# Optimization experiments

Hardware: AMD Instinct MI355X
Metric: run time of the kernel (lower is better)

The kernel has to match this reference:

```python
import jax, jax.numpy as jnp
import numpy as np

N_NODES = 50000
N_FEAT = 63          # nodeChannels C = N_FEAT + 1 = 64
N_EDGES = 800000
N_LABELS = 10000
BATCH = 4
N_LAYERS = 5
C = N_FEAT + 1


def setup_inputs() -> dict:
    key = jax.random.key(0)
    ks = jax.random.split(key, 16)
    s = 0.05  # small init scale for numerical sanity
    return {
        "cov": jax.random.normal(ks[0], (BATCH, N_LABELS), jnp.float32),
        "nodes": jax.random.normal(ks[1], (N_NODES, N_FEAT), jnp.float32),
        "edges": jax.random.randint(ks[2], (2, N_EDGES), 0, N_NODES, jnp.int64 if jax.config.jax_enable_x64 else jnp.int32),
        "count2label": jnp.arange(N_LABELS, dtype=jnp.int32),
        "ggc_weight": jax.random.normal(ks[3], (N_LAYERS, C, C), jnp.float32) * s,
        "gru_w_ih": jax.random.normal(ks[4], (3 * C, C), jnp.float32) * s,
        "gru_w_hh": jax.random.normal(ks[5], (3 * C, C), jnp.float32) * s,
        "gru_b_ih": jax.random.normal(ks[6], (3 * C,), jnp.float32) * s,
        "gru_b_hh": jax.random.normal(ks[7], (3 * C,), jnp.float32) * s,
        "ai_w": jax.random.normal(ks[8], (2 * C, 2 * C), jnp.float32) * s,
        "ai_b": jax.random.normal(ks[9], (2 * C,), jnp.float32) * s,
        "aj_w": jax.random.normal(ks[10], (2 * C, 2 * C), jnp.float32) * s,
        "aj_b": jax.random.normal(ks[11], (2 * C,), jnp.float32) * s,
        "mlp_w": jax.random.normal(ks[12], (256, 2 * C), jnp.float32) * s,
        "mlp_b": jax.random.normal(ks[13], (256,), jnp.float32) * s,
        "critic_w": jax.random.normal(ks[14], (1, 256), jnp.float32) * s,
        "critic_b": jax.random.normal(ks[15], (1,), jnp.float32) * s,
    }


def _gru_cell(m, h, w_ih, w_hh, b_ih, b_hh):
    # torch GRUCell, gate order r, z, n
    gx = m @ w_ih.T + b_ih   # [..., 3C]
    gh = h @ w_hh.T + b_hh
    c = h.shape[-1]
    xr, xz, xn = gx[..., :c], gx[..., c:2 * c], gx[..., 2 * c:]
    hr, hz, hn = gh[..., :c], gh[..., c:2 * c], gh[..., 2 * c:]
    r = jax.nn.sigmoid(xr + hr)
    z = jax.nn.sigmoid(xz + hz)
    n = jnp.tanh(xn + r * hn)
    return (1.0 - z) * n + z * h


def reference(cov, nodes, edges, count2label, ggc_weight,
              gru_w_ih, gru_w_hh, gru_b_ih, gru_b_hh,
              ai_w, ai_b, aj_w, aj_b, mlp_w, mlp_b, critic_w, critic_b):
    n, f = nodes.shape
    b = cov.shape[0]
    # scatter coverage into per-graph node channel: covInGraph[count2label] = cov
    cov_in_graph = jnp.zeros((b, n), cov.dtype).at[:, count2label].set(cov)
    # batched node input [B, N, C]; batched graph = B identical copies w/ offset edges
    x0 = jnp.concatenate(
        [jnp.broadcast_to(nodes, (b, n, f)), cov_in_graph[..., None]], axis=-1)
    src, dst = edges[0], edges[1]

    def scatter_add(mb):  # [N, C] -> [N, C]: sum messages from source at target
        return jax.ops.segment_sum(mb[src], dst, num_segments=n)

    x = x0
    for i in range(ggc_weight.shape[0]):
        m = x @ ggc_weight[i]                     # dense per-layer matmul [B,N,C]
        agg = jax.vmap(scatter_add)(m)            # edge scatter-add propagate
        x = _gru_cell(agg, x, gru_w_ih, gru_w_hh, gru_b_ih, gru_b_hh)

    # attention gate: sigmoid(Wi cat) * relu(Wj cat), cat = [x, x0]
    cat = jnp.concatenate([x, x0], axis=-1)       # [B, N, 2C]
    att = jax.nn.sigmoid(cat @ ai_w.T + ai_b) * jax.nn.relu(cat @ aj_w.T + aj_b)
    pooled = jax.nn.relu(att.sum(axis=1))         # global_add_pool -> [B, 2C]
    state = jax.nn.relu(pooled @ mlp_w.T + mlp_b) # graphmlp
    return state @ critic_w.T + critic_b          # critic value [B, 1]
```

## Files before the change

kernel.cpp:

```cpp
#include <hip/hip_runtime.h>
#include <math.h>

#define NN 50000
#define NF 63
#define NE 800000
#define NL 10000
#define NB 4
#define NLAY 5
#define BN (NB*NN)
#define NTILES (BN/64)
#define SCAN_NBLK ((NN+255)/256)
#define HIST_NBLK ((NE+255)/256)
#define X0_NBLK ((BN*16)/256)
#define COV_NBLK ((NB*NL+255)/256)

using f32x4  = __attribute__((ext_vector_type(4))) float;
using f32x2  = __attribute__((ext_vector_type(2))) float;
using bf16x8 = __attribute__((ext_vector_type(8))) __bf16;

__device__ __forceinline__ float frcp(float x){ return __builtin_amdgcn_rcpf(x); }
__device__ __forceinline__ float sigm(float v){ return frcp(1.f + __expf(-v)); }
__device__ __forceinline__ float tanh_f(float v){ return fmaf(-2.f, frcp(__expf(2.f*v) + 1.f), 1.f); }

__device__ __forceinline__ ushort f2bf(float f){
    uint u = __builtin_bit_cast(uint, f);
    u += 0x7fffu + ((u >> 16) & 1u);
    return (ushort)(u >> 16);
}
__device__ __forceinline__ float bf_lo(uint v){ return __builtin_bit_cast(float, v << 16); }
__device__ __forceinline__ float bf_hi(uint v){ return __builtin_bit_cast(float, v & 0xffff0000u); }
__device__ __forceinline__ float bfu(ushort v){ return __builtin_bit_cast(float, ((uint)v) << 16); }

__device__ __forceinline__ bf16x8 ldfrag(const ushort* p){
    uint4 v = *(const uint4*)p;
    return __builtin_bit_cast(bf16x8, v);
}
__device__ __forceinline__ f32x4 MFMA(bf16x8 a, bf16x8 b, f32x4 c){
    return __builtin_amdgcn_mfma_f32_16x16x32_bf16(a, b, c, 0, 0, 0);
}

__global__ void k_setup(const int* __restrict__ edges, int* __restrict__ cnt,
                        const float* __restrict__ wih, const float* __restrict__ whh,
                        const float* __restrict__ aiw, const float* __restrict__ ajw,
                        const float* __restrict__ ggc,
                        ushort* __restrict__ whhb, ushort* __restrict__ aiwb,
                        ushort* __restrict__ ajwb, ushort* __restrict__ wfb,
                        const float* __restrict__ nodes, ushort* __restrict__ x0I,
                        uchar* __restrict__ x0F){
    int bid = blockIdx.x;
    if (bid < HIST_NBLK){
        int e = bid*256 + threadIdx.x;
        if (e < NE) atomicAdd(&cnt[edges[NE + e]], 1);
        return;
    }
    if (bid < HIST_NBLK + 416){
        int i = (bid - HIST_NBLK)*256 + threadIdx.x;
        if (i < 12288)        whhb[i]        = f2bf(whh[i]);
        else if (i < 28672)   aiwb[i-12288]  = f2bf(aiw[i-12288]);
        else if (i < 45056)   ajwb[i-28672]  = f2bf(ajw[i-28672]);
        else if (i < 106496){
            int t = i - 45056;
            int lay = t / 12288;
            int rem = t % 12288;
            int n = rem >> 6, k = rem & 63;
            const float* W  = ggc + lay*4096 + k*64;
            const float* wr = wih + n*64;
            float s = 0.f;
            #pragma unroll 8
            for (int c = 0; c < 64; ++c) s = fmaf(W[c], wr[c], s);
            wfb[t] = f2bf(s);
        }
        return;
    }
    int f = (bid - HIST_NBLK - 416)*256 + threadIdx.x;
    int row = f >> 4, c4 = f & 15;
    int n = row % NN, b = row / NN;
    float v[4];
    #pragma unroll
    for (int i = 0; i < 4; ++i){
        int c = c4*4 + i;
        v[i] = (c < NF) ? nodes[(size_t)n*NF + c] : 0.f;
    }
    uint2 pk;
    pk.x = (uint)f2bf(v[0]) | ((uint)f2bf(v[1]) << 16);
    pk.y = (uint)f2bf(v[2]) | ((uint)f2bf(v[3]) << 16);
    *(uint2*)(x0I + ((size_t)n*4 + b)*64 + c4*4) = pk;
    if (b == 0){
        uint q = 0;
        q = (uint)__builtin_amdgcn_cvt_pk_fp8_f32(v[0], v[1], (int)q, false);
        q = (uint)__builtin_amdgcn_cvt_pk_fp8_f32(v[2], v[3], (int)q, true);
        *(uint*)(x0F + (size_t)n*64 + c4*4) = q;
    }
}

__global__ void k_scan1(const int* __restrict__ cnt, int* __restrict__ tmp, int* __restrict__ bsum,
                        const float* __restrict__ cov, const int* __restrict__ c2l,
                        ushort* __restrict__ x0I, ushort* __restrict__ covB){
    if (blockIdx.x >= SCAN_NBLK){
        int i = (blockIdx.x - SCAN_NBLK)*256 + threadIdx.x;
        if (i < NB*NL){
            int b = i / NL, j = i % NL;
            int nd = c2l[j];
            ushort vb = f2bf(cov[i]);
            x0I[((size_t)nd*4 + b)*64 + 63] = vb;
            covB[(size_t)nd*4 + b] = vb;
        }
        return;
    }
    __shared__ int sh[256];
    int tx = threadIdx.x, i = blockIdx.x*256 + tx;
    int v = (i < NN) ? cnt[i] : 0;
    sh[tx] = v; __syncthreads();
    for (int off = 1; off < 256; off <<= 1){
        int u = (tx >= off) ? sh[tx-off] : 0;
        __syncthreads();
        sh[tx] += u;
        __syncthreads();
    }
    int incl = sh[tx];
    if (i < NN) tmp[i] = incl - v;
    if (tx == 255) bsum[blockIdx.x] = incl;
}

__global__ void k_scan2(const int* __restrict__ bsum, int* __restrict__ boff){
    __shared__ int sh[256];
    int tx = threadIdx.x;
    int v = (tx < SCAN_NBLK) ? bsum[tx] : 0;
    sh[tx] = v; __syncthreads();
    for (int off = 1; off < 256; off <<= 1){
        int u = (tx >= off) ? sh[tx-off] : 0;
        __syncthreads();
        sh[tx] += u;
        __syncthreads();
    }
    boff[tx] = sh[tx] - v;
}

__global__ void k_scan3(const int* __restrict__ tmp, const int* __restrict__ boff,
                        int* __restrict__ row_start, int* __restrict__ cursor){
    int i = blockIdx.x*256 + threadIdx.x;
    if (i < NN){
        int rs = tmp[i] + boff[blockIdx.x];
        row_start[i] = rs;
        cursor[i] = rs;
    }
    if (i == 0) row_start[NN] = NE;
}

__global__ void k_fillcsr(const int* __restrict__ edges, int* __restrict__ cursor, int* __restrict__ csr_src){
    int e = blockIdx.x*256 + threadIdx.x;
    if (e < NE){
        int d = edges[NE + e];
        int pos = atomicAdd(&cursor[d], 1);
        csr_src[pos] = edges[e];
    }
}

__device__ __forceinline__ void gather0q(const uchar* __restrict__ x0F,
                                         const ushort* __restrict__ covB,
                                         const int* __restrict__ row_start,
                                         const int* __restrict__ csr_src,
                                         int d0, int l, ushort* __restrict__ sAgg,
                                         int rbase){
    const int qn = l >> 4, t = l & 15;
    const uint off = (uint)(t*4);
    const int d = d0 + qn;
    const int e0 = row_start[d], e1 = row_start[d+1];
    f32x2 a01 = (f32x2){0.f,0.f}, a23 = (f32x2){0.f,0.f};
    float c = 0.f;
    int e = e0;
    for (; e + 16 <= e1; e += 16){
        int s[16];
        #pragma unroll
        for (int j = 0; j < 16; ++j) s[j] = csr_src[e + j];
        uint v[16];
        #pragma unroll
        for (int j = 0; j < 16; ++j) v[j] = *(const uint*)(x0F + (size_t)s[j]*64 + off);
        #pragma unroll
        for (int j = 0; j < 16; ++j){
            a01 += __builtin_amdgcn_cvt_pk_f32_fp8(v[j], false);
            a23 += __builtin_amdgcn_cvt_pk_f32_fp8(v[j], true);
        }
        if (t < 4){
            #pragma unroll
            for (int j = 0; j < 16; ++j) c += bf_lo((uint)covB[(size_t)s[j]*4 + t]);
        }
    }
    if (e < e1){
        int s[16];
        #pragma unroll
        for (int j = 0; j < 16; ++j){ int ee = e + j; if (ee >= e1) ee = e1 - 1; s[j] = csr_src[ee]; }
        uint v[16];
        #pragma unroll
        for (int j = 0; j < 16; ++j){
            v[j] = *(const uint*)(x0F + (size_t)s[j]*64 + off);
            if (e + j >= e1) v[j] = 0u;
        }
        #pragma unroll
        for (int j = 0; j < 16; ++j){
            a01 += __builtin_amdgcn_cvt_pk_f32_fp8(v[j], false);
            a23 += __builtin_amdgcn_cvt_pk_f32_fp8(v[j], true);
        }
        if (t < 4){
            #pragma unroll
            for (int j = 0; j < 16; ++j){
                float cv = bf_lo((uint)covB[(size_t)s[j]*4 + t]);
                c += (e + j < e1) ? cv : 0.f;
            }
        }
    }
    uint2 pk;
    pk.x = (uint)f2bf(a01.x) | ((uint)f2bf(a01.y) << 16);
    pk.y = (uint)f2bf(a23.x) | ((uint)f2bf(a23.y) << 16);
    #pragma unroll
    for (int b = 0; b < 4; ++b){
        float cb = __shfl(c, (l & 48) | b);
        uint2 o = pk;
        if (t == 15) o.y = (o.y & 0xffffu) | ((uint)f2bf(cb) << 16);
        *(uint2*)(&sAgg[(size_t)(rbase + qn*4 + b)*72 + t*4]) = o;
    }
}

__device__ __forceinline__ void gather4q(const uchar* __restrict__ xF,
                                         const int* __restrict__ row_start,
                                         const int* __restrict__ csr_src,
                                         int d0, int l, ushort* __restrict__ sAgg,
                                         int rbase){
    const int qn = l >> 4;
    const int t  = l & 15;
    const uint off = (uint)(t*16);
    const int d = d0 + qn;
    const int e0 = row_start[d], e1 = row_start[d+1];
    f32x2 ac[8];
    #pragma unroll
    for (int k = 0; k < 8; ++k) ac[k] = (f32x2){0.f,0.f};

    int e = e0;
    for (; e + 16 <= e1; e += 16){
        int s[16];
        #pragma unroll
        for (int j = 0; j < 16; ++j) s[j] = csr_src[e + j];
        uint4 v[16];
        #pragma unroll
        for (int j = 0; j < 16; ++j) v[j] = *(const uint4*)(xF + (size_t)s[j]*256 + off);
        #pragma unroll
        for (int j = 0; j < 16; ++j){
            ac[0] += __builtin_amdgcn_cvt_pk_f32_fp8(v[j].x, false);
            ac[1] += __builtin_amdgcn_cvt_pk_f32_fp8(v[j].x, true);
            ac[2] += __builtin_amdgcn_cvt_pk_f32_fp8(v[j].y, false);
            ac[3] += __builtin_amdgcn_cvt_pk_f32_fp8(v[j].y, true);
            ac[4] += __builtin_amdgcn_cvt_pk_f32_fp8(v[j].z, false);
            ac[5] += __builtin_amdgcn_cvt_pk_f32_fp8(v[j].z, true);
            ac[6] += __builtin_amdgcn_cvt_pk_f32_fp8(v[j].w, false);
            ac[7] += __builtin_amdgcn_cvt_pk_f32_fp8(v[j].w, true);
        }
    }
    if (e < e1){
        int s[16];
        #pragma unroll
        for (int j = 0; j < 16; ++j){ int ee = e + j; if (ee >= e1) ee = e1 - 1; s[j] = csr_src[ee]; }
        uint4 v[16];
        #pragma unroll
        for (int j = 0; j < 16; ++j){
            v[j] = *(const uint4*)(xF + (size_t)s[j]*256 + off);
            if (e + j >= e1) v[j] = (uint4){0u,0u,0u,0u};
        }
        #pragma unroll
        for (int j = 0; j < 16; ++j){
            ac[0] += __builtin_amdgcn_cvt_pk_f32_fp8(v[j].x, false);
            ac[1] += __builtin_amdgcn_cvt_pk_f32_fp8(v[j].x, true);
            ac[2] += __builtin_amdgcn_cvt_pk_f32_fp8(v[j].y, false);
            ac[3] += __builtin_amdgcn_cvt_pk_f32_fp8(v[j].y, true);
            ac[4] += __builtin_amdgcn_cvt_pk_f32_fp8(v[j].z, false);
            ac[5] += __builtin_amdgcn_cvt_pk_f32_fp8(v[j].z, true);
            ac[6] += __builtin_amdgcn_cvt_pk_f32_fp8(v[j].w, false);
            ac[7] += __builtin_amdgcn_cvt_pk_f32_fp8(v[j].w, true);
        }
    }

    const int row = rbase + qn*4 + (t >> 2);
    const int c0  = (t & 3)*16;
    uint4 o0, o1;
    o0.x = (uint)f2bf(ac[0].x) | ((uint)f2bf(ac[0].y) << 16);
    o0.y = (uint)f2bf(ac[1].x) | ((uint)f2bf(ac[1].y) << 16);
    o0.z = (uint)f2bf(ac[2].x) | ((uint)f2bf(ac[2].y) << 16);
    o0.w = (uint)f2bf(ac[3].x) | ((uint)f2bf(ac[3].y) << 16);
    o1.x = (uint)f2bf(ac[4].x) | ((uint)f2bf(ac[4].y) << 16);
    o1.y = (uint)f2bf(ac[5].x) | ((uint)f2bf(ac[5].y) << 16);
    o1.z = (uint)f2bf(ac[6].x) | ((uint)f2bf(ac[6].y) << 16);
    o1.w = (uint)f2bf(ac[7].x) | ((uint)f2bf(ac[7].y) << 16);
    *(uint4*)(&sAgg[(size_t)row*72 + c0])     = o0;
    *(uint4*)(&sAgg[(size_t)row*72 + c0 + 8]) = o1;
}

__device__ __forceinline__ void gru_core(const ushort* sAgg, const ushort* sX,
                                         const ushort* __restrict__ wfb, const ushort* __restrict__ whhb,
                                         const float* __restrict__ bih, const float* __restrict__ bhh,
                                         int li, int q, int n0, float xv[4][4]){
    f32x4 Cr[4], Cz[4], Cxn[4], Chn[4];
    #pragma unroll
    for (int m = 0; m < 4; ++m){
        Cr[m]=(f32x4){0.f,0.f,0.f,0.f}; Cz[m]=(f32x4){0.f,0.f,0.f,0.f};
        Cxn[m]=(f32x4){0.f,0.f,0.f,0.f}; Chn[m]=(f32x4){0.f,0.f,0.f,0.f};
    }
    __builtin_amdgcn_s_setprio(1);
    #pragma unroll
    for (int ks = 0; ks < 4; ++ks){
        const ushort* wb = (ks < 2) ? wfb : whhb;
        const ushort* sT = (ks < 2) ? sAgg : sX;
        const int kb = (ks & 1)*32;
        bf16x8 Br = ldfrag(wb + (size_t)(n0 + li)*64 + kb + q*8);
        bf16x8 Bz = ldfrag(wb + (size_t)(64 + n0 + li)*64 + kb + q*8);
        bf16x8 Bn = ldfrag(wb + (size_t)(128 + n0 + li)*64 + kb + q*8);
        #pragma unroll
        for (int m = 0; m < 4; ++m){
            bf16x8 A = ldfrag(&sT[(m*16 + li)*72 + kb + q*8]);
            Cr[m] = MFMA(A, Br, Cr[m]);
            Cz[m] = MFMA(A, Bz, Cz[m]);
            if (ks < 2) Cxn[m] = MFMA(A, Bn, Cxn[m]);
            else        Chn[m] = MFMA(A, Bn, Chn[m]);
        }
    }
    __builtin_amdgcn_s_setprio(0);
    const int c = n0 + li;
    const float br_ = bih[c]     + bhh[c];
    const float bz_ = bih[64+c]  + bhh[64+c];
    const float bn_ = bih[128+c];
    const float bh_ = bhh[128+c];
    #pragma unroll
    for (int m = 0; m < 4; ++m){
        #pragma unroll
        for (int rg = 0; rg < 4; ++rg){
            int rl = m*16 + q*4 + rg;
            float r = sigm(Cr[m][rg] + br_);
            float z = sigm(Cz[m][rg] + bz_);
            float nng = tanh_f(Cxn[m][rg] + bn_ + r*(Chn[m][rg] + bh_));
            xv[m][rg] = (1.f - z)*nng + z*bfu(sX[rl*72 + c]);
        }
    }
}

__device__ __forceinline__ void store_state(ushort* sAgg, int tx, int w, int li, int q,
                                            const float xv[4][4], int R0,
                                            ushort* __restrict__ xout, uchar* __restrict__ xFout){
    __syncthreads();
    const int c = 16*w + li;
    #pragma unroll
    for (int m = 0; m < 4; ++m)
        #pragma unroll
        for (int rg = 0; rg < 4; ++rg)
            sAgg[(m*16 + q*4 + rg)*72 + c] = f2bf(xv[m][rg]);
    __syncthreads();
    #pragma unroll
    for (int it = 0; it < 2; ++it){
        int idx = it*256 + tx, r = idx >> 3, g = idx & 7;
        *(uint4*)(xout + (size_t)(R0 + r)*64 + g*8) = *(const uint4*)(&sAgg[r*72 + g*8]);
    }
    {
        int r = tx >> 2, g = tx & 3;
        const ushort* src = &sAgg[r*72 + g*16];
        uint4 a = *(const uint4*)src;
        uint4 b = *(const uint4*)(src + 8);
        uint4 o; uint qd;
        qd = (uint)__builtin_amdgcn_cvt_pk_fp8_f32(bf_lo(a.x), bf_hi(a.x), 0, false);
        qd = (uint)__builtin_amdgcn_cvt_pk_fp8_f32(bf_lo(a.y), bf_hi(a.y), (int)qd, true);
        o.x = qd;
        qd = (uint)__builtin_amdgcn_cvt_pk_fp8_f32(bf_lo(a.z), bf_hi(a.z), 0, false);
        qd = (uint)__builtin_amdgcn_cvt_pk_fp8_f32(bf_lo(a.w), bf_hi(a.w), (int)qd, true);
        o.y = qd;
        qd = (uint)__builtin_amdgcn_cvt_pk_fp8_f32(bf_lo(b.x), bf_hi(b.x), 0, false);
        qd = (uint)__builtin_amdgcn_cvt_pk_fp8_f32(bf_lo(b.y), bf_hi(b.y), (int)qd, true);
        o.z = qd;
        qd = (uint)__builtin_amdgcn_cvt_pk_fp8_f32(bf_lo(b.z), bf_hi(b.z), 0, false);
        qd = (uint)__builtin_amdgcn_cvt_pk_fp8_f32(bf_lo(b.w), bf_hi(b.w), (int)qd, true);
        o.w = qd;
        *(uint4*)(xFout + (size_t)(R0 + r)*64 + g*16) = o;
    }
}

__global__ __launch_bounds__(256, 4) void k_gru0f(const uchar* __restrict__ x0F,
                                               const ushort* __restrict__ covB,
                                               const int* __restrict__ row_start,
                                               const int* __restrict__ csr_src,
                                               const ushort* __restrict__ x0I,
                                               const ushort* __restrict__ wfb, const ushort* __restrict__ whhb,
                                               const float* __restrict__ bih, const float* __restrict__ bhh,
                                               ushort* __restrict__ xout, uchar* __restrict__ xFout){
    __shared__ __align__(16) ushort sAgg[64*72];
    __shared__ __align__(16) ushort sX[64*72];
    const int tx = threadIdx.x;
    const int l  = tx & 63, li = l & 15, q = l >> 4;
    const int w  = __builtin_amdgcn_readfirstlane(tx >> 6);
    const int R0 = blockIdx.x*64;

    #pragma unroll
    for (int it = 0; it < 2; ++it){
        int idx = it*256 + tx, r = idx >> 3, g = idx & 7;
        *(uint4*)(&sX[r*72 + g*8]) = *(const uint4*)(x0I + (size_t)(R0 + r)*64 + g*8);
    }
    gather0q(x0F, covB, row_start, csr_src, blockIdx.x*16 + w*4, l, sAgg, w*16);
    __syncthreads();

    float xv[4][4];
    gru_core(sAgg, sX, wfb, whhb, bih, bhh, li, q, 16*w, xv);
    store_state(sAgg, tx, w, li, q, xv, R0, xout, xFout);
}

__global__ __launch_bounds__(256, 4) void k_gruFf(const uchar* __restrict__ xFin,
                                               const int* __restrict__ row_start,
                                               const int* __restrict__ csr_src,
                                               const ushort* __restrict__ xsrc,
                                               const ushort* __restrict__ wfb, const ushort* __restrict__ whhb,
                                               const float* __restrict__ bih, const float* __restrict__ bhh,
                                               ushort* __restrict__ xout, uchar* __restrict__ xFout){
    __shared__ __align__(16) ushort sAgg[64*72];
    __shared__ __align__(16) ushort sX[64*72];
    const int tx = threadIdx.x;
    const int l  = tx & 63, li = l & 15, q = l >> 4;
    const int w  = __builtin_amdgcn_readfirstlane(tx >> 6);
    const int R0 = blockIdx.x*64;

    #pragma unroll
    for (int it = 0; it < 2; ++it){
        int idx = it*256 + tx, r = idx >> 3, g = idx & 7;
        *(uint4*)(&sX[r*72 + g*8]) = *(const uint4*)(xsrc + (size_t)(R0 + r)*64 + g*8);
    }
    gather4q(xFin, row_start, csr_src, blockIdx.x*16 + w*4, l, sAgg, w*16);
    __syncthreads();

    float xv[4][4];
    gru_core(sAgg, sX, wfb, whhb, bih, bhh, li, q, 16*w, xv);
    store_state(sAgg, tx, w, li, q, xv, R0, xout, xFout);
}

__global__ __launch_bounds__(256, 4) void k_gruLf(const uchar* __restrict__ xFin,
                                               const int* __restrict__ row_start,
                                               const int* __restrict__ csr_src,
                                               const ushort* __restrict__ xsrc,
                                               const ushort* __restrict__ wfb, const ushort* __restrict__ whhb,
                                               const float* __restrict__ bih, const float* __restrict__ bhh,
                                               const ushort* __restrict__ x0I,
                                               const ushort* __restrict__ aiwb, const float* __restrict__ aib,
                                               const ushort* __restrict__ ajwb, const float* __restrict__ ajb,
                                               float* __restrict__ pooled16){
    __shared__ __align__(16) ushort sAgg[64*72];
    __shared__ __align__(16) ushort sX[64*72];
    const int tx = threadIdx.x;
    const int l  = tx & 63, li = l & 15, q = l >> 4;
    const int w  = __builtin_amdgcn_readfirstlane(tx >> 6);
    const int R0 = blockIdx.x*64;

    #pragma unroll
    for (int it = 0; it < 2; ++it){
        int idx = it*256 + tx, r = idx >> 3, g = idx & 7;
        *(uint4*)(&sX[r*72 + g*8]) = *(const uint4*)(xsrc + (size_t)(R0 + r)*64 + g*8);
    }
    gather4q(xFin, row_start, csr_src, blockIdx.x*16 + w*4, l, sAgg, w*16);
    __syncthreads();

    float xv[4][4];
    gru_core(sAgg, sX, wfb, whhb, bih, bhh, li, q, 16*w, xv);
    __syncthreads();

    const int c = 16*w + li;
    #pragma unroll
    for (int m = 0; m < 4; ++m)
        #pragma unroll
        for (int rg = 0; rg < 4; ++rg)
            sAgg[(m*16 + q*4 + rg)*72 + c] = f2bf(xv[m][rg]);
    #pragma unroll
    for (int it = 0; it < 2; ++it){
        int idx = it*256 + tx, r = idx >> 3, g = idx & 7;
        *(uint4*)(&sX[r*72 + g*8]) = *(const uint4*)(x0I + (size_t)(R0 + r)*64 + g*8);
    }
    __syncthreads();

    f32x4 Ai[2][4], Aj[2][4];
    #pragma unroll
    for (int t = 0; t < 2; ++t)
        #pragma unroll
        for (int m = 0; m < 4; ++m){ Ai[t][m]=(f32x4){0.f,0.f,0.f,0.f}; Aj[t][m]=(f32x4){0.f,0.f,0.f,0.f}; }

    const int nb0 = 32*w;
    __builtin_amdgcn_s_setprio(1);
    #pragma unroll
    for (int ks = 0; ks < 4; ++ks){
        const ushort* sT = (ks < 2) ? sAgg : sX;
        const int kb = (ks & 1)*32;
        bf16x8 Bi[2], Bj[2];
        #pragma unroll
        for (int t = 0; t < 2; ++t){
            Bi[t] = ldfrag(aiwb + (size_t)(nb0 + 16*t + li)*128 + ks*32 + q*8);
            Bj[t] = ldfrag(ajwb + (size_t)(nb0 + 16*t + li)*128 + ks*32 + q*8);
        }
        #pragma unroll
        for (int m = 0; m < 4; ++m){
            bf16x8 A = ldfrag(&sT[(m*16 + li)*72 + kb + q*8]);
            #pragma unroll
            for (int t = 0; t < 2; ++t){
                Ai[t][m] = MFMA(A, Bi[t], Ai[t][m]);
                Aj[t][m] = MFMA(A, Bj[t], Aj[t][m]);
            }
        }
    }
    __builtin_amdgcn_s_setprio(0);

    float* pb = pooled16 + (size_t)(blockIdx.x & 15)*512;
    #pragma unroll
    for (int t = 0; t < 2; ++t){
        int cc = nb0 + 16*t + li;
        float bia = aib[cc], bja = ajb[cc];
        float vs[4] = {0.f, 0.f, 0.f, 0.f};
        #pragma unroll
        for (int m = 0; m < 4; ++m){
            #pragma unroll
            for (int rg = 0; rg < 4; ++rg){
                float s = sigm(Ai[t][m][rg] + bia);
                float a = Aj[t][m][rg] + bja;
                a = a > 0.f ? a : 0.f;
                vs[rg] += s*a;
            }
        }
        #pragma unroll
        for (int b = 0; b < 4; ++b){
            vs[b] += __shfl_xor(vs[b], 16);
            vs[b] += __shfl_xor(vs[b], 32);
        }
        if (l < 16){
            #pragma unroll
            for (int b = 0; b < 4; ++b) atomicAdd(&pb[b*128 + nb0 + 16*t + l], vs[b]);
        }
    }
}

__global__ void k_final(const float* __restrict__ pooled16, const float* __restrict__ mw,
                        const float* __restrict__ mb, const float* __restrict__ cw,
                        const float* __restrict__ cb, float* __restrict__ out){
    __shared__ float red[256];
    int t = threadIdx.x;
    int b = blockIdx.x;
    float acc = mb[t];
    #pragma unroll 4
    for (int k = 0; k < 128; ++k){
        float p = 0.f;
        #pragma unroll
        for (int kb = 0; kb < 16; ++kb) p += pooled16[kb*512 + b*128 + k];
        p = p > 0.f ? p : 0.f;
        acc = fmaf(p, mw[t*128 + k], acc);
    }
    float st = acc > 0.f ? acc : 0.f;
    red[t] = st * cw[t];
    __syncthreads();
    for (int off = 128; off > 0; off >>= 1){
        if (t < off) red[t] += red[t + off];
        __syncthreads();
    }
    if (t == 0) out[b] = red[0] + cb[0];
}

extern "C" void kernel_launch(void* const* d_in, const int* in_sizes, int n_in,
                              void* d_out, int out_size, void* d_ws, size_t ws_size,
                              hipStream_t stream) {
    const float* cov   = (const float*)d_in[0];
    const float* nodes = (const float*)d_in[1];
    const int*   edges = (const int*)d_in[2];
    const int*   c2l   = (const int*)d_in[3];
    const float* ggc   = (const float*)d_in[4];
    const float* wih   = (const float*)d_in[5];
    const float* whh   = (const float*)d_in[6];
    const float* bih   = (const float*)d_in[7];
    const float* bhh   = (const float*)d_in[8];
    const float* aiw   = (const float*)d_in[9];
    const float* aib   = (const float*)d_in[10];
    const float* ajw   = (const float*)d_in[11];
    const float* ajb   = (const float*)d_in[12];
    const float* mlpw  = (const float*)d_in[13];
    const float* mlpb  = (const float*)d_in[14];
    const float* cw    = (const float*)d_in[15];
    const float* cb    = (const float*)d_in[16];
    float* out = (float*)d_out;

    const size_t XSZ = (size_t)BN * 64;
    float* ws = (float*)d_ws;
    float* pooled16 = ws;
    ushort* xS    = (ushort*)(pooled16 + 8192);
    ushort* x0I   = xS + XSZ;
    ushort* aggx  = x0I + XSZ;
    ushort* covB  = aggx + XSZ;
    ushort* whhb  = covB + (size_t)NN*4;
    ushort* aiwb  = whhb + 12288;
    ushort* ajwb  = aiwb + 16384;
    ushort* wfb   = ajwb + 16384;
    uchar* xF     = (uchar*)(wfb + 61440);
    uchar* x0F    = xF + XSZ;
    int* cnt       = (int*)(x0F + (size_t)NN*64);
    int* tmp       = cnt + NN;
    int* bsum      = tmp + NN;
    int* boff      = bsum + 256;
    int* row_start = boff + 256;
    int* cursor    = row_start + (NN + 1);
    int* csr_src   = cursor + NN;

    hipMemsetAsync(cnt, 0, (size_t)NN*sizeof(int), stream);
    hipMemsetAsync(pooled16, 0, 8192*sizeof(float), stream);
    hipMemsetAsync(covB, 0, (size_t)NN*4*sizeof(ushort), stream);

    k_setup<<<HIST_NBLK + 416 + X0_NBLK, 256, 0, stream>>>(edges, cnt, wih, whh, aiw, ajw, ggc,
                                                           whhb, aiwb, ajwb, wfb,
                                                           nodes, x0I, x0F);
    k_scan1<<<SCAN_NBLK + COV_NBLK, 256, 0, stream>>>(cnt, tmp, bsum, cov, c2l, x0I, covB);
    k_scan2<<<1, 256, 0, stream>>>(bsum, boff);
    k_scan3<<<SCAN_NBLK, 256, 0, stream>>>(tmp, boff, row_start, cursor);
    k_fillcsr<<<(NE + 255)/256, 256, 0, stream>>>(edges, cursor, csr_src);

    uchar* xFbuf[2] = { xF, (uchar*)aggx };

    for (int i = 0; i < NLAY; ++i){
        const ushort* wf = wfb + (size_t)i*12288;
        if (i == 0){
            k_gru0f<<<NTILES, 256, 0, stream>>>(x0F, covB, row_start, csr_src, x0I,
                                                wf, whhb, bih, bhh, xS, xFbuf[0]);
        } else if (i < NLAY - 1){
            k_gruFf<<<NTILES, 256, 0, stream>>>(xFbuf[(i+1)&1], row_start, csr_src, xS,
                                                wf, whhb, bih, bhh, xS, xFbuf[i&1]);
        } else {
            k_gruLf<<<NTILES, 256, 0, stream>>>(xFbuf[(i+1)&1], row_start, csr_src, xS,
                                                wf, whhb, bih, bhh,
                                                x0I, aiwb, aib, ajwb, ajb, pooled16);
        }
    }

    k_final<<<NB, 256, 0, stream>>>(pooled16, mlpw, mlpb, cw, cb, out);
    (void)in_sizes; (void)n_in; (void)out_size; (void)ws_size;
}
```

Measured before the change: 490.1 us.

## Double-buffer edge gathers, merge scan kernels, write fp8 state directly from registers

The neighbor gather loop now works in chunks of 8 edges with two register buffers, so the next chunk's loads are issued before the current chunk is converted. This is meant to hide gather latency and cut register pressure compared with the old 16-wide batches. The scan2 kernel is folded into scan3, with each block recomputing the block-offset prefix, which removes one launch. The state store now quantizes to fp8 straight from fp32 registers into a new shared buffer instead of re-reading bf16 from shared memory. That adds 4 KB of LDS per block and changes rounding slightly, since there is no longer a bf16 step before fp8. Row bounds are also loaded earlier in the kernels.

```diff
diff --git a/kernel.cpp b/kernel.cpp
--- a/kernel.cpp
+++ b/kernel.cpp
@@ -28,8 +28,12 @@
     return (ushort)(u >> 16);
 }
 __device__ __forceinline__ float bf_lo(uint v){ return __builtin_bit_cast(float, v << 16); }
-__device__ __forceinline__ float bf_hi(uint v){ return __builtin_bit_cast(float, v & 0xffff0000u); }
 __device__ __forceinline__ float bfu(ushort v){ return __builtin_bit_cast(float, ((uint)v) << 16); }
+
+__device__ __forceinline__ uchar f2fp8(float v){
+    int enc = __builtin_amdgcn_cvt_pk_fp8_f32(v, v, 0, false);
+    return (uchar)(enc & 0xff);
+}
 
 __device__ __forceinline__ bf16x8 ldfrag(const ushort* p){
     uint4 v = *(const uint4*)p;
@@ -122,7 +126,8 @@
     if (tx == 255) bsum[blockIdx.x] = incl;
 }
 
-__global__ void k_scan2(const int* __restrict__ bsum, int* __restrict__ boff){
+__global__ void k_scan3(const int* __restrict__ tmp, const int* __restrict__ bsum,
+                        int* __restrict__ row_start, int* __restrict__ cursor){
     __shared__ int sh[256];
     int tx = threadIdx.x;
     int v = (tx < SCAN_NBLK) ? bsum[tx] : 0;
@@ -133,14 +138,10 @@
         sh[tx] += u;
         __syncthreads();
     }
-    boff[tx] = sh[tx] - v;
-}
-
-__global__ void k_scan3(const int* __restrict__ tmp, const int* __restrict__ boff,
-                        int* __restrict__ row_start, int* __restrict__ cursor){
-    int i = blockIdx.x*256 + threadIdx.x;
+    int boff = sh[blockIdx.x] - bsum[blockIdx.x];
+    int i = blockIdx.x*256 + tx;
     if (i < NN){
-        int rs = tmp[i] + boff[blockIdx.x];
+        int rs = tmp[i] + boff;
         row_start[i] = rs;
         cursor[i] = rs;
     }
@@ -158,14 +159,11 @@
 
 __device__ __forceinline__ void gather0q(const uchar* __restrict__ x0F,
                                          const ushort* __restrict__ covB,
-                                         const int* __restrict__ row_start,
                                          const int* __restrict__ csr_src,
-                                         int d0, int l, ushort* __restrict__ sAgg,
-                                         int rbase){
+                                         int e0, int e1, int l,
+                                         ushort* __restrict__ sAgg, int rbase){
     const int qn = l >> 4, t = l & 15;
     const uint off = (uint)(t*4);
-    const int d = d0 + qn;
-    const int e0 = row_start[d], e1 = row_start[d+1];
     f32x2 a01 = (f32x2){0.f,0.f}, a23 = (f32x2){0.f,0.f};
     float c = 0.f;
     int e = e0;
@@ -221,60 +219,57 @@
     }
 }
 
+__device__ __forceinline__ void load8(uint4 v[8], const uchar* __restrict__ xF,
+                                      const int* __restrict__ csr_src,
+                                      int eb, int e1, uint off){
+    #pragma unroll
+    for (int j = 0; j < 8; ++j){
+        int ee = eb + j; if (ee >= e1) ee = e1 - 1;
+        int s = csr_src[ee];
+        v[j] = *(const uint4*)(xF + (size_t)s*256 + off);
+    }
+}
+__device__ __forceinline__ void conv8(const uint4 v[8], int eb, int e1, f32x2 ac[8]){
+    #pragma unroll
+    for (int j = 0; j < 8; ++j){
+        uint4 x = v[j];
+        if (eb + j >= e1) x = (uint4){0u,0u,0u,0u};
+        ac[0] += __builtin_amdgcn_cvt_pk_f32_fp8(x.x, false);
+        ac[1] += __builtin_amdgcn_cvt_pk_f32_fp8(x.x, true);
+        ac[2] += __builtin_amdgcn_cvt_pk_f32_fp8(x.y, false);
+        ac[3] += __builtin_amdgcn_cvt_pk_f32_fp8(x.y, true);
+        ac[4] += __builtin_amdgcn_cvt_pk_f32_fp8(x.z, false);
+        ac[5] += __builtin_amdgcn_cvt_pk_f32_fp8(x.z, true);
+        ac[6] += __builtin_amdgcn_cvt_pk_f32_fp8(x.w, false);
+        ac[7] += __builtin_amdgcn_cvt_pk_f32_fp8(x.w, true);
+    }
+}
+
 __device__ __forceinline__ void gather4q(const uchar* __restrict__ xF,
-                                         const int* __restrict__ row_start,
                                          const int* __restrict__ csr_src,
-                                         int d0, int l, ushort* __restrict__ sAgg,
-                                         int rbase){
+                                         int e0, int e1, int l,
+                                         ushort* __restrict__ sAgg, int rbase){
     const int qn = l >> 4;
     const int t  = l & 15;
     const uint off = (uint)(t*16);
-    const int d = d0 + qn;
-    const int e0 = row_start[d], e1 = row_start[d+1];
     f32x2 ac[8];
     #pragma unroll
     for (int k = 0; k < 8; ++k) ac[k] = (f32x2){0.f,0.f};
 
-    int e = e0;
-    for (; e + 16 <= e1; e += 16){
-        int s[16];
-        #pragma unroll
-        for (int j = 0; j < 16; ++j) s[j] = csr_src[e + j];
-        uint4 v[16];
-        #pragma unroll
-        for (int j = 0; j < 16; ++j) v[j] = *(const uint4*)(xF + (size_t)s[j]*256 + off);
-        #pragma unroll
-        for (int j = 0; j < 16; ++j){
-            ac[0] += __builtin_amdgcn_cvt_pk_f32_fp8(v[j].x, false);
-            ac[1] += __builtin_amdgcn_cvt_pk_f32_fp8(v[j].x, true);
-            ac[2] += __builtin_amdgcn_cvt_pk_f32_fp8(v[j].y, false);
-            ac[3] += __builtin_amdgcn_cvt_pk_f32_fp8(v[j].y, true);
-            ac[4] += __builtin_amdgcn_cvt_pk_f32_fp8(v[j].z, false);
-            ac[5] += __builtin_amdgcn_cvt_pk_f32_fp8(v[j].z, true);
-            ac[6] += __builtin_amdgcn_cvt_pk_f32_fp8(v[j].w, false);
-            ac[7] += __builtin_amdgcn_cvt_pk_f32_fp8(v[j].w, true);
-        }
-    }
-    if (e < e1){
-        int s[16];
-        #pragma unroll
-        for (int j = 0; j < 16; ++j){ int ee = e + j; if (ee >= e1) ee = e1 - 1; s[j] = csr_src[ee]; }
-        uint4 v[16];
-        #pragma unroll
-        for (int j = 0; j < 16; ++j){
-            v[j] = *(const uint4*)(xF + (size_t)s[j]*256 + off);
-            if (e + j >= e1) v[j] = (uint4){0u,0u,0u,0u};
-        }
-        #pragma unroll
-        for (int j = 0; j < 16; ++j){
-            ac[0] += __builtin_amdgcn_cvt_pk_f32_fp8(v[j].x, false);
-            ac[1] += __builtin_amdgcn_cvt_pk_f32_fp8(v[j].x, true);
-            ac[2] += __builtin_amdgcn_cvt_pk_f32_fp8(v[j].y, false);
-            ac[3] += __builtin_amdgcn_cvt_pk_f32_fp8(v[j].y, true);
-            ac[4] += __builtin_amdgcn_cvt_pk_f32_fp8(v[j].z, false);
-            ac[5] += __builtin_amdgcn_cvt_pk_f32_fp8(v[j].z, true);
-            ac[6] += __builtin_amdgcn_cvt_pk_f32_fp8(v[j].w, false);
-            ac[7] += __builtin_amdgcn_cvt_pk_f32_fp8(v[j].w, true);
+    uint4 va[8], vb[8];
+    int eb = e0;
+    if (eb < e1){
+        load8(va, xF, csr_src, eb, e1, off);
+        while (true){
+            int ebB = eb + 8;
+            if (ebB >= e1){ conv8(va, eb, e1, ac); break; }
+            load8(vb, xF, csr_src, ebB, e1, off);
+            conv8(va, eb, e1, ac);
+            int ebA = ebB + 8;
+            if (ebA >= e1){ conv8(vb, ebB, e1, ac); break; }
+            load8(va, xF, csr_src, ebA, e1, off);
+            conv8(vb, ebB, e1, ac);
+            eb = ebA;
         }
     }
 
@@ -340,7 +335,7 @@
     }
 }
 
-__device__ __forceinline__ void store_state(ushort* sAgg, int tx, int w, int li, int q,
+__device__ __forceinline__ void store_state(ushort* sAgg, uchar* sF8, int tx, int w, int li, int q,
                                             const float xv[4][4], int R0,
                                             ushort* __restrict__ xout, uchar* __restrict__ xFout){
     __syncthreads();
@@ -348,8 +343,11 @@
     #pragma unroll
     for (int m = 0; m < 4; ++m)
         #pragma unroll
-        for (int rg = 0; rg < 4; ++rg)
-            sAgg[(m*16 + q*4 + rg)*72 + c] = f2bf(xv[m][rg]);
+        for (int rg = 0; rg < 4; ++rg){
+            int r = m*16 + q*4 + rg;
+            sAgg[r*72 + c] = f2bf(xv[m][rg]);
+            sF8[r*64 + c]  = f2fp8(xv[m][rg]);
+        }
     __syncthreads();
     #pragma unroll
     for (int it = 0; it < 2; ++it){
@@ -358,23 +356,7 @@
     }
     {
         int r = tx >> 2, g = tx & 3;
-        const ushort* src = &sAgg[r*72 + g*16];
-        uint4 a = *(const uint4*)src;
-        uint4 b = *(const uint4*)(src + 8);
-        uint4 o; uint qd;
-        qd = (uint)__builtin_amdgcn_cvt_pk_fp8_f32(bf_lo(a.x), bf_hi(a.x), 0, false);
-        qd = (uint)__builtin_amdgcn_cvt_pk_fp8_f32(bf_lo(a.y), bf_hi(a.y), (int)qd, true);
-        o.x = qd;
-        qd = (uint)__builtin_amdgcn_cvt_pk_fp8_f32(bf_lo(a.z), bf_hi(a.z), 0, false);
-        qd = (uint)__builtin_amdgcn_cvt_pk_fp8_f32(bf_lo(a.w), bf_hi(a.w), (int)qd, true);
-        o.y = qd;
-        qd = (uint)__builtin_amdgcn_cvt_pk_fp8_f32(bf_lo(b.x), bf_hi(b.x), 0, false);
-        qd = (uint)__builtin_amdgcn_cvt_pk_fp8_f32(bf_lo(b.y), bf_hi(b.y), (int)qd, true);
-        o.z = qd;
-        qd = (uint)__builtin_amdgcn_cvt_pk_fp8_f32(bf_lo(b.z), bf_hi(b.z), 0, false);
-        qd = (uint)__builtin_amdgcn_cvt_pk_fp8_f32(bf_lo(b.w), bf_hi(b.w), (int)qd, true);
-        o.w = qd;
-        *(uint4*)(xFout + (size_t)(R0 + r)*64 + g*16) = o;
+        *(uint4*)(xFout + (size_t)(R0 + r)*64 + g*16) = *(const uint4*)(&sF8[r*64 + g*16]);
     }
 }
 
@@ -388,22 +370,25 @@
                                                ushort* __restrict__ xout, uchar* __restrict__ xFout){
     __shared__ __align__(16) ushort sAgg[64*72];
     __shared__ __align__(16) ushort sX[64*72];
+    __shared__ __align__(16) uchar  sF8[64*64];
     const int tx = threadIdx.x;
     const int l  = tx & 63, li = l & 15, q = l >> 4;
     const int w  = __builtin_amdgcn_readfirstlane(tx >> 6);
     const int R0 = blockIdx.x*64;
+    const int d  = blockIdx.x*16 + w*4 + (l >> 4);
+    const int e0 = row_start[d], e1 = row_start[d+1];
 
     #pragma unroll
     for (int it = 0; it < 2; ++it){
         int idx = it*256 + tx, r = idx >> 3, g = idx & 7;
         *(uint4*)(&sX[r*72 + g*8]) = *(const uint4*)(x0I + (size_t)(R0 + r)*64 + g*8);
     }
-    gather0q(x0F, covB, row_start, csr_src, blockIdx.x*16 + w*4, l, sAgg, w*16);
+    gather0q(x0F, covB, csr_src, e0, e1, l, sAgg, w*16);
     __syncthreads();
 
     float xv[4][4];
     gru_core(sAgg, sX, wfb, whhb, bih, bhh, li, q, 16*w, xv);
-    store_state(sAgg, tx, w, li, q, xv, R0, xout, xFout);
+    store_state(sAgg, sF8, tx, w, li, q, xv, R0, xout, xFout);
 }
 
 __global__ __launch_bounds__(256, 4) void k_gruFf(const uchar* __restrict__ xFin,
@@ -415,22 +400,25 @@
                                                ushort* __restrict__ xout, uchar* __restrict__ xFout){
     __shared__ __align__(16) ushort sAgg[64*72];
     __shared__ __align__(16) ushort sX[64*72];
+    __shared__ __align__(16) uchar  sF8[64*64];
     const int tx = threadIdx.x;
     const int l  = tx & 63, li = l & 15, q = l >> 4;
     const int w  = __builtin_amdgcn_readfirstlane(tx >> 6);
     const int R0 = blockIdx.x*64;
+    const int d  = blockIdx.x*16 + w*4 + (l >> 4);
+    const int e0 = row_start[d], e1 = row_start[d+1];
 
     #pragma unroll
     for (int it = 0; it < 2; ++it){
         int idx = it*256 + tx, r = idx >> 3, g = idx & 7;
         *(uint4*)(&sX[r*72 + g*8]) = *(const uint4*)(xsrc + (size_t)(R0 + r)*64 + g*8);
     }
-    gather4q(xFin, row_start, csr_src, blockIdx.x*16 + w*4, l, sAgg, w*16);
+    gather4q(xFin, csr_src, e0, e1, l, sAgg, w*16);
     __syncthreads();
 
     float xv[4][4];
     gru_core(sAgg, sX, wfb, whhb, bih, bhh, li, q, 16*w, xv);
-    store_state(sAgg, tx, w, li, q, xv, R0, xout, xFout);
+    store_state(sAgg, sF8, tx, w, li, q, xv, R0, xout, xFout);
 }
 
 __global__ __launch_bounds__(256, 4) void k_gruLf(const uchar* __restrict__ xFin,
@@ -449,13 +437,15 @@
     const int l  = tx & 63, li = l & 15, q = l >> 4;
     const int w  = __builtin_amdgcn_readfirstlane(tx >> 6);
     const int R0 = blockIdx.x*64;
+    const int d  = blockIdx.x*16 + w*4 + (l >> 4);
+    const int e0 = row_start[d], e1 = row_start[d+1];
 
     #pragma unroll
     for (int it = 0; it < 2; ++it){
         int idx = it*256 + tx, r = idx >> 3, g = idx & 7;
         *(uint4*)(&sX[r*72 + g*8]) = *(const uint4*)(xsrc + (size_t)(R0 + r)*64 + g*8);
     }
-    gather4q(xFin, row_start, csr_src, blockIdx.x*16 + w*4, l, sAgg, w*16);
+    gather4q(xFin, csr_src, e0, e1, l, sAgg, w*16);
     __syncthreads();
 
     float xv[4][4];
@@ -609,8 +599,7 @@
                                                            whhb, aiwb, ajwb, wfb,
                                                            nodes, x0I, x0F);
     k_scan1<<<SCAN_NBLK + COV_NBLK, 256, 0, stream>>>(cnt, tmp, bsum, cov, c2l, x0I, covB);
-    k_scan2<<<1, 256, 0, stream>>>(bsum, boff);
-    k_scan3<<<SCAN_NBLK, 256, 0, stream>>>(tmp, boff, row_start, cursor);
+    k_scan3<<<SCAN_NBLK, 256, 0, stream>>>(tmp, bsum, row_start, cursor);
     k_fillcsr<<<(NE + 255)/256, 256, 0, stream>>>(edges, cursor, csr_src);
 
     uchar* xFbuf[2] = { xF, (uchar*)aggx };
```

Result: slower. 505.8 us (+3.2%).
